# Optimization experiments

Measured on AMD Instinct MI355X. Metric: run time of the kernel, lower is better.

## Reference

```python
import jax, jax.numpy as jnp
import numpy as np

N, D = 8192, 1024


def setup_inputs() -> dict:
    key = jax.random.key(0)
    k1, k2, k3 = jax.random.split(key, 3)
    f_1 = jax.random.normal(k1, (N, D), dtype=jnp.float32)
    f_2 = jax.random.normal(k2, (N, D), dtype=jnp.float32)
    f_3 = jax.random.normal(k3, (N, D), dtype=jnp.float32)
    return {"f_1": f_1, "f_2": f_2, "f_3": f_3, "batch": 3}


def _svdvals(x):
    # torch.svd computes full U, S, V; only singular values are consumed.
    return jnp.linalg.svd(x, compute_uv=False)


def reference(f_1, f_2, f_3, batch):
    if batch == 2:
        s_1 = _svdvals(f_1)
        if f_2.shape[0] == 0:
            return s_1[0] ** 2
        s_2 = _svdvals(f_2)
        return s_1.mean() + s_2.mean()
    elif batch == 3:
        s_1 = _svdvals(f_1)
        s_2 = _svdvals(f_2)
        s_3 = _svdvals(f_3)
        return s_1[0] ** 2 + 0.5 * (s_2[0] ** 2 + s_3[0] ** 2)
```

## Files before the change

kernel.cpp:

```cpp
#include <hip/hip_runtime.h>


#define DIM 1024
#define NROW 8192
#define MSZ (DIM*DIM)
#define NS 5

typedef __attribute__((ext_vector_type(8))) short short8;
typedef __attribute__((ext_vector_type(4))) float f32x4;

__device__ inline float bf2f(unsigned short u) {
    union { unsigned i; float f; } x; x.i = ((unsigned)u) << 16; return x.f;
}
__device__ inline unsigned short f2bf(float f) {
    union { float f; unsigned i; } x; x.f = f;
    unsigned r = x.i + 0x7FFFu + ((x.i >> 16) & 1u);
    return (unsigned short)(r >> 16);
}
__device__ inline void gload16(const void* g, void* l) {
    __builtin_amdgcn_global_load_lds(
        (const __attribute__((address_space(1))) unsigned int*)g,
        (__attribute__((address_space(3))) unsigned int*)l, 16, 0, 0);
}

__global__ __launch_bounds__(256)
void tconv_k(const float* __restrict__ f0, const float* __restrict__ f1,
             const float* __restrict__ f2, unsigned short* __restrict__ ft) {
    const int m = blockIdx.z;
    const float* f = (m == 0) ? f0 : (m == 1 ? f1 : f2);
    unsigned short* o = ft + (size_t)m * DIM * NROW;
    __shared__ float T[64][68];
    const int c0 = blockIdx.x * 64, r0 = blockIdx.y * 64;
    const int tid = threadIdx.x;
    const int cx = (tid & 15) * 4, ry = tid >> 4;
#pragma unroll
    for (int i = 0; i < 4; ++i) {
        int r = ry + i * 16;
        float4 v = *(const float4*)&f[(size_t)(r0 + r) * DIM + c0 + cx];
        T[cx + 0][r] = v.x;
        T[cx + 1][r] = v.y;
        T[cx + 2][r] = v.z;
        T[cx + 3][r] = v.w;
    }
    __syncthreads();
#pragma unroll
    for (int i = 0; i < 4; ++i) {
        int c = ry + i * 16;
        float4 g = *(const float4*)&T[c][cx];
        ushort4 u;
        u.x = f2bf(g.x); u.y = f2bf(g.y); u.z = f2bf(g.z); u.w = f2bf(g.w);
        *(ushort4*)&o[(size_t)(c0 + c) * NROW + r0 + cx] = u;
    }
}

__global__ __launch_bounds__(256)
void syrk_sk(const unsigned short* __restrict__ src, float* __restrict__ Gp) {
    const int b = blockIdx.x;
    const int ky = b & 3;
    const int q = b >> 2;
    const int m = q / 36;
    const int tile = q - m * 36;
    int idx = tile, ti = 0;
    while (idx >= 8 - ti) { idx -= 8 - ti; ++ti; }
    const int tj = ti + idx;
    const int i0 = ti * 128, j0 = tj * 128;
    const unsigned short* S = src + (size_t)m * DIM * NROW;
    float* G = Gp + ((size_t)m * 36 + tile) * 16384;
    const int k0b = ky << 11;

    __shared__ unsigned short As0[2 * 128 * 32];
    __shared__ unsigned short Bs0[2 * 128 * 32];
    __shared__ unsigned short As1[2 * 128 * 32];
    __shared__ unsigned short Bs1[2 * 128 * 32];

    const int tid = threadIdx.x, w = tid >> 6, lane = tid & 63;
    const int wi = w >> 1, wj = w & 1;

    f32x4 acc[4][4];
#pragma unroll
    for (int a = 0; a < 4; ++a)
#pragma unroll
        for (int c = 0; c < 4; ++c) acc[a][c] = (f32x4){0.f, 0.f, 0.f, 0.f};

    const int lr = lane >> 2;
    const int ksw = (((lane & 3) ^ ((lane >> 4) & 3)) * 8);
    const int fr = lane & 15;
    const int slot = (((lane >> 4) ^ ((fr >> 2) & 3)) * 8);

#define STAGE(AS, BS, KK)                                                     \
    _Pragma("unroll")                                                         \
    for (int h = 0; h < 2; ++h)                                               \
        _Pragma("unroll")                                                     \
        for (int p = 0; p < 2; ++p) {                                         \
            int rr = w * 32 + p * 16;                                         \
            gload16(S + (size_t)(i0 + rr + lr) * NROW + (KK) + h * 32 + ksw,  \
                    &(AS)[h * 4096 + rr * 32]);                               \
            gload16(S + (size_t)(j0 + rr + lr) * NROW + (KK) + h * 32 + ksw,  \
                    &(BS)[h * 4096 + rr * 32]);                               \
        }

#define COMPUTE(AS, BS)                                                       \
    _Pragma("unroll")                                                         \
    for (int h = 0; h < 2; ++h) {                                             \
        short8 af[4], bfv[4];                                                 \
        _Pragma("unroll")                                                     \
        for (int a = 0; a < 4; ++a)                                           \
            af[a] = *(const short8*)&(AS)[h * 4096 + (wi * 64 + a * 16 + fr) * 32 + slot]; \
        _Pragma("unroll")                                                     \
        for (int c = 0; c < 4; ++c)                                           \
            bfv[c] = *(const short8*)&(BS)[h * 4096 + (wj * 64 + c * 16 + fr) * 32 + slot]; \
        _Pragma("unroll")                                                     \
        for (int a = 0; a < 4; ++a)                                           \
            _Pragma("unroll")                                                 \
            for (int c = 0; c < 4; ++c)                                       \
                acc[a][c] = __builtin_amdgcn_mfma_f32_16x16x32_bf16(          \
                    af[a], bfv[c], acc[a][c], 0, 0, 0);                       \
    }

    STAGE(As0, Bs0, k0b)
    __syncthreads();

    int k0 = k0b;
#pragma unroll 1
    for (int t = 0; t < 15; ++t) {
        STAGE(As1, Bs1, k0 + 64)
        COMPUTE(As0, Bs0)
        __syncthreads();
        STAGE(As0, Bs0, k0 + 128)
        COMPUTE(As1, Bs1)
        __syncthreads();
        k0 += 128;
    }
    STAGE(As1, Bs1, k0 + 64)
    COMPUTE(As0, Bs0)
    __syncthreads();
    COMPUTE(As1, Bs1)

#undef STAGE
#undef COMPUTE

    const int qr = (lane >> 4) * 4, cn = lane & 15;
#pragma unroll
    for (int a = 0; a < 4; ++a)
#pragma unroll
        for (int c = 0; c < 4; ++c) {
            int cl = wj * 64 + c * 16 + cn;
#pragma unroll
            for (int reg = 0; reg < 4; ++reg) {
                int rl = wi * 64 + a * 16 + qr + reg;
                atomicAdd(&G[rl * 128 + cl], acc[a][c][reg]);
            }
        }
}

__global__ __launch_bounds__(256)
void convert_k(const float* __restrict__ Gp, float* __restrict__ trout,
               unsigned short* __restrict__ dst) {
    const int m = blockIdx.z;
    int idx = blockIdx.x, ti = 0;
    while (idx >= 8 - ti) { idx -= 8 - ti; ++ti; }
    const int tj = ti + idx;
    const int i0 = ti * 128, j0 = tj * 128;
    const float* G = Gp + ((size_t)m * 36 + blockIdx.x) * 16384;
    unsigned short* D = dst + (size_t)m * MSZ;
    __shared__ unsigned short T[128][136];
    const int tid = threadIdx.x;
    const int cx = (tid & 31) * 4, ry = tid >> 5;
    float dtr = 0.f;
#pragma unroll 4
    for (int t = 0; t < 16; ++t) {
        int r = ry + t * 8;
        float4 g = *(const float4*)&G[r * 128 + cx];
        ushort4 o;
        o.x = f2bf(g.x); o.y = f2bf(g.y); o.z = f2bf(g.z); o.w = f2bf(g.w);
        *(ushort4*)&D[(size_t)(i0 + r) * DIM + j0 + cx] = o;
        int rs = r ^ (cx & 124);
        T[cx + 0][rs] = o.x; T[cx + 1][rs] = o.y;
        T[cx + 2][rs] = o.z; T[cx + 3][rs] = o.w;
        if (ti == tj) {
            int d = r - cx;
            if (d >= 0 && d < 4)
                dtr += (d == 0 ? g.x : d == 1 ? g.y : d == 2 ? g.z : g.w);
        }
    }
    if (ti == tj) atomicAdd(&trout[m], dtr);
    if (ti != tj) {
        __syncthreads();
#pragma unroll 4
        for (int t = 0; t < 16; ++t) {
            int p = ry + t * 8;
            int qs = cx ^ (p & 124);
            ushort4 o = *(const ushort4*)&T[p][qs];
            *(ushort4*)&D[(size_t)(j0 + p) * DIM + i0 + cx] = o;
        }
    }
}

__global__ __launch_bounds__(256)
void sq_k(const unsigned short* __restrict__ src, const float* __restrict__ trin,
          float* __restrict__ trout, unsigned short* __restrict__ dst) {
    const int m = blockIdx.z;
    const unsigned short* S = src + (size_t)m * MSZ;
    unsigned short* D = dst + (size_t)m * MSZ;
    int idx = blockIdx.x, ti = 0;
    while (idx >= 16 - ti) { idx -= 16 - ti; ++ti; }
    const int tj = ti + idx;
    const int i0 = ti * 64, j0 = tj * 64;
    float tv = trin[m];
    const float sc = 1.f / (tv * tv);

    __shared__ unsigned short As0[2 * 64 * 32];
    __shared__ unsigned short Bs0[2 * 64 * 32];
    __shared__ unsigned short As1[2 * 64 * 32];
    __shared__ unsigned short Bs1[2 * 64 * 32];
    __shared__ unsigned short Ts[64][68];

    const int tid = threadIdx.x, w = tid >> 6, lane = tid & 63;
    const int wi = w >> 1, wj = w & 1;
    f32x4 acc[2][2];
#pragma unroll
    for (int a = 0; a < 2; ++a)
#pragma unroll
        for (int b = 0; b < 2; ++b) acc[a][b] = (f32x4){0.f, 0.f, 0.f, 0.f};

    const int lr = lane >> 2;
    const int ksw = (((lane & 3) ^ ((lane >> 4) & 3)) * 8);
    const int fr = lane & 15;
    const int slot = (((lane >> 4) ^ ((fr >> 2) & 3)) * 8);

#define SQ_STAGE(AS, BS, KK)                                                  \
    _Pragma("unroll")                                                         \
    for (int h = 0; h < 2; ++h) {                                             \
        gload16(S + (size_t)(i0 + w * 16 + lr) * DIM + (KK) + h * 32 + ksw,   \
                &(AS)[h * 2048 + w * 16 * 32]);                               \
        gload16(S + (size_t)(j0 + w * 16 + lr) * DIM + (KK) + h * 32 + ksw,   \
                &(BS)[h * 2048 + w * 16 * 32]);                               \
    }

#define SQ_COMPUTE(AS, BS)                                                    \
    _Pragma("unroll")                                                         \
    for (int h = 0; h < 2; ++h) {                                             \
        short8 af[2], bfv[2];                                                 \
        _Pragma("unroll")                                                     \
        for (int a = 0; a < 2; ++a)                                           \
            af[a] = *(const short8*)&(AS)[h * 2048 + (wi * 32 + a * 16 + fr) * 32 + slot]; \
        _Pragma("unroll")                                                     \
        for (int c = 0; c < 2; ++c)                                           \
            bfv[c] = *(const short8*)&(BS)[h * 2048 + (wj * 32 + c * 16 + fr) * 32 + slot]; \
        _Pragma("unroll")                                                     \
        for (int a = 0; a < 2; ++a)                                           \
            _Pragma("unroll")                                                 \
            for (int c = 0; c < 2; ++c)                                       \
                acc[a][c] = __builtin_amdgcn_mfma_f32_16x16x32_bf16(          \
                    af[a], bfv[c], acc[a][c], 0, 0, 0);                       \
    }

    SQ_STAGE(As0, Bs0, 0)
    __syncthreads();

    int k0 = 0;
#pragma unroll 1
    for (int t = 0; t < 7; ++t) {
        SQ_STAGE(As1, Bs1, k0 + 64)
        SQ_COMPUTE(As0, Bs0)
        __syncthreads();
        SQ_STAGE(As0, Bs0, k0 + 128)
        SQ_COMPUTE(As1, Bs1)
        __syncthreads();
        k0 += 128;
    }
    SQ_STAGE(As1, Bs1, k0 + 64)
    SQ_COMPUTE(As0, Bs0)
    __syncthreads();
    SQ_COMPUTE(As1, Bs1)

#undef SQ_STAGE
#undef SQ_COMPUTE

    const int qr = (lane >> 4) * 4, cn = lane & 15;
#pragma unroll
    for (int a = 0; a < 2; ++a)
#pragma unroll
        for (int b = 0; b < 2; ++b) {
            int cl = wj * 32 + b * 16 + cn;
#pragma unroll
            for (int reg = 0; reg < 4; ++reg) {
                int rl = wi * 32 + a * 16 + qr + reg;
                unsigned short val = f2bf(acc[a][b][reg] * sc);
                D[(size_t)(i0 + rl) * DIM + j0 + cl] = val;
                Ts[cl][rl] = val;
            }
        }
    if (ti == tj && wi == wj) {
        int d = cn - qr;
        if (d >= 0 && d < 4)
            atomicAdd(&trout[m], (acc[0][0][d] + acc[1][1][d]) * sc);
    }
    if (ti != tj) {
        __syncthreads();
        const int cx = (tid & 15) * 4, ry = tid >> 4;
#pragma unroll
        for (int tq = 0; tq < 4; ++tq) {
            int p = ry + tq * 16;
            ushort4 o;
            o.x = Ts[p][cx + 0]; o.y = Ts[p][cx + 1];
            o.z = Ts[p][cx + 2]; o.w = Ts[p][cx + 3];
            *(ushort4*)&D[(size_t)(j0 + p) * DIM + i0 + cx] = o;
        }
    }
}

__global__ __launch_bounds__(256)
void mv_bf16(const unsigned short* __restrict__ M, const float* __restrict__ vin,
             float* __restrict__ vout) {
    int m = blockIdx.y;
    const unsigned short* A = M + (size_t)m * MSZ;
    int wv = threadIdx.x >> 6, lane = threadIdx.x & 63;
    int row = blockIdx.x * 4 + wv;
    const unsigned short* a = A + (size_t)row * DIM;
    float s = 0.f;
    if (vin) {
        const float* v = vin + m * DIM;
#pragma unroll
        for (int jb = 0; jb < DIM; jb += 512) {
            int j = jb + lane * 8;
            short8 x = *(const short8*)&a[j];
#pragma unroll
            for (int u = 0; u < 8; ++u)
                s += bf2f((unsigned short)x[u]) * v[j + u];
        }
    } else {
#pragma unroll
        for (int jb = 0; jb < DIM; jb += 512) {
            int j = jb + lane * 8;
            short8 x = *(const short8*)&a[j];
#pragma unroll
            for (int u = 0; u < 8; ++u)
                s += bf2f((unsigned short)x[u]);
        }
    }
    for (int off = 32; off; off >>= 1) s += __shfl_down(s, off);
    if (lane == 0) vout[m * DIM + row] = s;
}

__global__ __launch_bounds__(256)
void ray_k(const float* __restrict__ Gp, const float* __restrict__ wv,
           float* __restrict__ num) {
    const int m = blockIdx.y;
    int idx = blockIdx.x, ti = 0;
    while (idx >= 8 - ti) { idx -= 8 - ti; ++ti; }
    const int tj = ti + idx;
    const float* G = Gp + ((size_t)m * 36 + blockIdx.x) * 16384;
    const float* wi = wv + m * DIM + ti * 128;
    const float* wj = wv + m * DIM + tj * 128;
    const int tid = threadIdx.x;
    const int r = tid >> 1, c0 = (tid & 1) * 64;
    float inner = 0.f;
    const float4* g4 = (const float4*)&G[r * 128 + c0];
    const float4* w4 = (const float4*)&wj[c0];
#pragma unroll
    for (int t = 0; t < 16; ++t) {
        float4 g = g4[t], ww = w4[t];
        inner += g.x * ww.x + g.y * ww.y + g.z * ww.z + g.w * ww.w;
    }
    float s = wi[r] * inner;
    for (int off = 32; off; off >>= 1) s += __shfl_down(s, off);
    __shared__ float part[4];
    int lane = tid & 63, wx = tid >> 6;
    if (lane == 0) part[wx] = s;
    __syncthreads();
    if (tid == 0) {
        float tot = part[0] + part[1] + part[2] + part[3];
        if (ti != tj) tot *= 2.f;
        atomicAdd(&num[m], tot);
    }
}

__global__ __launch_bounds__(256)
void final_k(const float* __restrict__ num, const float* __restrict__ w,
             float* __restrict__ out) {
    __shared__ float red[256];
    int tid = threadIdx.x;
    float lam[3];
    for (int m = 0; m < 3; ++m) {
        float s = 0.f;
        for (int i = tid; i < DIM; i += 256) { float x = w[m * DIM + i]; s += x * x; }
        red[tid] = s; __syncthreads();
        for (int off = 128; off; off >>= 1) {
            if (tid < off) red[tid] += red[tid + off];
            __syncthreads();
        }
        lam[m] = num[m] / red[0]; __syncthreads();
    }
    if (tid == 0) out[0] = lam[0] + 0.5f * (lam[1] + lam[2]);
}

extern "C" void kernel_launch(void* const* d_in, const int* in_sizes, int n_in,
                              void* d_out, int out_size, void* d_ws, size_t ws_size,
                              hipStream_t stream) {
    const float* f0 = (const float*)d_in[0];
    const float* f1 = (const float*)d_in[1];
    const float* f2 = (const float*)d_in[2];

    char* base = (char*)d_ws;
    unsigned short* ft = (unsigned short*)base;
    unsigned short* Q  = (unsigned short*)base;
    unsigned short* P  = (unsigned short*)(base + 50331648);
    float* G32 = (float*)(base + 56623104);
    float* trbuf = (float*)(base + 63700992);
    float* num = trbuf + 40;
    float* v = (float*)(base + 63701248);
    float* w = v + 3 * DIM;

    hipMemsetAsync(G32, 0, 7078144, stream);

    dim3 gt(DIM / 64, NROW / 64, 3);
    tconv_k<<<gt, 256, 0, stream>>>(f0, f1, f2, ft);

    syrk_sk<<<432, 256, 0, stream>>>(ft, G32);
    convert_k<<<dim3(36, 1, 3), 256, 0, stream>>>(G32, trbuf, P);

    unsigned short* cur = P;
    unsigned short* nxt = Q;
    for (int s = 0; s < NS; ++s) {
        sq_k<<<dim3(136, 1, 3), 256, 0, stream>>>(cur, trbuf + s * 3,
                                                  trbuf + (s + 1) * 3, nxt);
        unsigned short* t2 = cur; cur = nxt; nxt = t2;
    }

    dim3 b(256, 1, 1);
    dim3 gm(DIM / 4, 3, 1);
    mv_bf16<<<gm, b, 0, stream>>>(cur, nullptr, v);
    mv_bf16<<<gm, b, 0, stream>>>(cur, v, w);

    ray_k<<<dim3(36, 3, 1), 256, 0, stream>>>(G32, w, num);
    final_k<<<1, 256, 0, stream>>>(num, w, (float*)d_out);
}
```

Measured before the change: 268.7 us.

## Replace double-buffered K=64 staging with a 4-stage K=32 LDS ring

Splits the shared-memory tiles into four 32-wide K buffers used as a rotating ring, so three stages of global-to-LDS loads stay in flight while one is computed. Explicit s_waitcnt vmcnt plus raw s_barrier replace __syncthreads, waiting only for the oldest stage. The goal is to hide global load latency in the SYRK kernel better. In exchange there are twice as many barrier points per unit of K, less MFMA work between barriers, and hand-counted vmcnt values that must stay correct.

```diff
diff --git a/kernel.cpp b/kernel.cpp
--- a/kernel.cpp
+++ b/kernel.cpp
@@ -68,10 +68,10 @@
     float* G = Gp + ((size_t)m * 36 + tile) * 16384;
     const int k0b = ky << 11;
 
-    __shared__ unsigned short As0[2 * 128 * 32];
-    __shared__ unsigned short Bs0[2 * 128 * 32];
-    __shared__ unsigned short As1[2 * 128 * 32];
-    __shared__ unsigned short Bs1[2 * 128 * 32];
+    __shared__ unsigned short As0[128 * 32], As1[128 * 32],
+                              As2[128 * 32], As3[128 * 32];
+    __shared__ unsigned short Bs0[128 * 32], Bs1[128 * 32],
+                              Bs2[128 * 32], Bs3[128 * 32];
 
     const int tid = threadIdx.x, w = tid >> 6, lane = tid & 63;
     const int wi = w >> 1, wj = w & 1;
@@ -87,28 +87,25 @@
     const int fr = lane & 15;
     const int slot = (((lane >> 4) ^ ((fr >> 2) & 3)) * 8);
 
-#define STAGE(AS, BS, KK)                                                     \
+#define STAGE(I, KK)                                                          \
     _Pragma("unroll")                                                         \
-    for (int h = 0; h < 2; ++h)                                               \
-        _Pragma("unroll")                                                     \
-        for (int p = 0; p < 2; ++p) {                                         \
-            int rr = w * 32 + p * 16;                                         \
-            gload16(S + (size_t)(i0 + rr + lr) * NROW + (KK) + h * 32 + ksw,  \
-                    &(AS)[h * 4096 + rr * 32]);                               \
-            gload16(S + (size_t)(j0 + rr + lr) * NROW + (KK) + h * 32 + ksw,  \
-                    &(BS)[h * 4096 + rr * 32]);                               \
-        }
-
-#define COMPUTE(AS, BS)                                                       \
-    _Pragma("unroll")                                                         \
-    for (int h = 0; h < 2; ++h) {                                             \
+    for (int p = 0; p < 2; ++p) {                                             \
+        int rr = w * 32 + p * 16;                                             \
+        gload16(S + (size_t)(i0 + rr + lr) * NROW + (KK) + ksw,               \
+                &As##I[rr * 32]);                                             \
+        gload16(S + (size_t)(j0 + rr + lr) * NROW + (KK) + ksw,               \
+                &Bs##I[rr * 32]);                                             \
+    }
+
+#define COMPUTE(I)                                                            \
+    {                                                                         \
         short8 af[4], bfv[4];                                                 \
         _Pragma("unroll")                                                     \
         for (int a = 0; a < 4; ++a)                                           \
-            af[a] = *(const short8*)&(AS)[h * 4096 + (wi * 64 + a * 16 + fr) * 32 + slot]; \
+            af[a] = *(const short8*)&As##I[(wi * 64 + a * 16 + fr) * 32 + slot]; \
         _Pragma("unroll")                                                     \
         for (int c = 0; c < 4; ++c)                                           \
-            bfv[c] = *(const short8*)&(BS)[h * 4096 + (wj * 64 + c * 16 + fr) * 32 + slot]; \
+            bfv[c] = *(const short8*)&Bs##I[(wj * 64 + c * 16 + fr) * 32 + slot]; \
         _Pragma("unroll")                                                     \
         for (int a = 0; a < 4; ++a)                                           \
             _Pragma("unroll")                                                 \
@@ -117,27 +114,45 @@
                     af[a], bfv[c], acc[a][c], 0, 0, 0);                       \
     }
 
-    STAGE(As0, Bs0, k0b)
-    __syncthreads();
-
-    int k0 = k0b;
+#define ROUND(CI, SI, KK, VM)                                                 \
+    STAGE(SI, KK)                                                             \
+    asm volatile("s_waitcnt vmcnt(" #VM ")" ::: "memory");                    \
+    __builtin_amdgcn_s_barrier();                                             \
+    COMPUTE(CI)                                                               \
+    __builtin_amdgcn_s_barrier();
+
+#define ROUND_NOSTAGE(CI, VM)                                                 \
+    asm volatile("s_waitcnt vmcnt(" #VM ")" ::: "memory");                    \
+    __builtin_amdgcn_s_barrier();                                             \
+    COMPUTE(CI)                                                               \
+    __builtin_amdgcn_s_barrier();
+
+    STAGE(0, k0b)
+    STAGE(1, k0b + 32)
+    STAGE(2, k0b + 64)
+
+    int kk = k0b;
 #pragma unroll 1
-    for (int t = 0; t < 15; ++t) {
-        STAGE(As1, Bs1, k0 + 64)
-        COMPUTE(As0, Bs0)
-        __syncthreads();
-        STAGE(As0, Bs0, k0 + 128)
-        COMPUTE(As1, Bs1)
-        __syncthreads();
-        k0 += 128;
-    }
-    STAGE(As1, Bs1, k0 + 64)
-    COMPUTE(As0, Bs0)
-    __syncthreads();
-    COMPUTE(As1, Bs1)
+    for (int tb = 0; tb < 14; ++tb) {
+        ROUND(0, 3, kk + 96, 12)
+        ROUND(1, 0, kk + 128, 12)
+        ROUND(2, 1, kk + 160, 12)
+        ROUND(3, 2, kk + 192, 12)
+        kk += 128;
+    }
+    ROUND(0, 3, kk + 96, 12)
+    ROUND(1, 0, kk + 128, 12)
+    ROUND(2, 1, kk + 160, 12)
+    ROUND(3, 2, kk + 192, 12)
+    ROUND(0, 3, kk + 224, 12)
+    ROUND_NOSTAGE(1, 8)
+    ROUND_NOSTAGE(2, 4)
+    ROUND_NOSTAGE(3, 0)
 
 #undef STAGE
 #undef COMPUTE
+#undef ROUND
+#undef ROUND_NOSTAGE
 
     const int qr = (lane >> 4) * 4, cn = lane & 15;
 #pragma unroll
```

Measured after the change: 266.3 us. No clear change (-0.9%).
